# Optimization experiments

Hardware: AMD Instinct MI355X
Metric: run time of the kernel (lower is better)

The kernel has to match this reference:

```python
import jax, jax.numpy as jnp
import numpy as np

TAU = 1.0
K_TAU = 1.0
MAX_K = 64


def setup_inputs() -> dict:
    key = jax.random.key(0)
    ks = jax.random.split(key, 6)
    B, S, D, H = 8, 4096, 1024, 2048
    token_embeddings = jax.random.normal(ks[0], (B, S, D), dtype=jnp.float32)
    W1 = jax.random.normal(ks[1], (D, H), dtype=jnp.float32) * (1.0 / np.sqrt(D))
    b1 = jnp.zeros((H,), dtype=jnp.float32)
    W2 = jax.random.normal(ks[2], (H, 1), dtype=jnp.float32) * (1.0 / np.sqrt(H))
    b2 = jnp.zeros((1,), dtype=jnp.float32)
    k_logits = jax.random.normal(ks[3], (MAX_K,), dtype=jnp.float32) * 0.02
    return {"token_embeddings": token_embeddings, "W1": W1, "b1": b1,
            "W2": W2, "b2": b2, "k_logits": k_logits}


def _gumbel(rng, shape):
    u = jax.random.uniform(rng, shape, minval=1e-08, maxval=1.0 - 1e-08)
    return -jnp.log(-jnp.log(u))


def reference(token_embeddings, W1, b1, W2, b2, k_logits):
    B, S, D = token_embeddings.shape
    # scorer: Dense -> relu -> Dense(1), squeeze -> [B, S]
    h = jax.nn.relu(jnp.einsum('bsd,dh->bsh', token_embeddings, W1) + b1)
    importance_logits = (jnp.einsum('bsh,ho->bso', h, W2) + b2)[..., 0]

    rng = jax.random.key(42)  # training rng
    rng1, rng2 = jax.random.split(rng)

    # learnable-k selection (training branch)
    k_gumbel = _gumbel(rng1, k_logits.shape)
    k_soft = jax.nn.softmax((k_logits + k_gumbel) / K_TAU)
    expected_k = jnp.sum(k_soft * jnp.arange(1, MAX_K + 1, dtype=k_soft.dtype))
    k_selected = jnp.argmax(k_soft) + 1  # traced int scalar

    # gumbel-softmax hard top-k over tokens
    perturbed = importance_logits + _gumbel(rng2, importance_logits.shape)
    soft_mask = jax.nn.softmax(perturbed / TAU, axis=-1)  # [B, S]
    # rank of each token (0 = smallest); top-k == rank >= S - k
    rank = jnp.argsort(jnp.argsort(soft_mask, axis=-1), axis=-1)
    hard_mask = (rank >= S - k_selected).astype(soft_mask.dtype)
    selection_mask = jax.lax.stop_gradient(hard_mask - soft_mask) + soft_mask

    filtered_embeddings = token_embeddings * selection_mask[..., None]
    return filtered_embeddings, selection_mask, expected_k
```

## Files before the change

kernel.cpp:

```cpp
#include <hip/hip_runtime.h>
#include <stdint.h>

#define B_BATCH 8
#define S_SEQ   4096
#define D_DIM   1024
#define H_DIM   2048
#define M_TOK   (B_BATCH * S_SEQ)
#define MAXK    64
#define NSPLIT  2

typedef unsigned int u32;
typedef unsigned short u16;
typedef unsigned long long u64;
typedef __attribute__((ext_vector_type(8))) short short8;
typedef __attribute__((ext_vector_type(4))) float f32x4;

#define GLOBAL_AS __attribute__((address_space(1)))
#define LDS_AS    __attribute__((address_space(3)))


#define TF_ROUND(x0, x1, r) { x0 += x1; x1 = ((x1 << r) | (x1 >> (32 - r))); x1 ^= x0; }

__device__ __forceinline__ void tf2x32(u32 k0, u32 k1, u32 x0, u32 x1, u32& o0, u32& o1) {
  u32 k2 = k0 ^ k1 ^ 0x1BD11BDAu;
  x0 += k0; x1 += k1;
  TF_ROUND(x0, x1, 13) TF_ROUND(x0, x1, 15) TF_ROUND(x0, x1, 26) TF_ROUND(x0, x1, 6)
  x0 += k1; x1 += k2 + 1u;
  TF_ROUND(x0, x1, 17) TF_ROUND(x0, x1, 29) TF_ROUND(x0, x1, 16) TF_ROUND(x0, x1, 24)
  x0 += k2; x1 += k0 + 2u;
  TF_ROUND(x0, x1, 13) TF_ROUND(x0, x1, 15) TF_ROUND(x0, x1, 26) TF_ROUND(x0, x1, 6)
  x0 += k0; x1 += k1 + 3u;
  TF_ROUND(x0, x1, 17) TF_ROUND(x0, x1, 29) TF_ROUND(x0, x1, 16) TF_ROUND(x0, x1, 24)
  x0 += k1; x1 += k2 + 4u;
  TF_ROUND(x0, x1, 13) TF_ROUND(x0, x1, 15) TF_ROUND(x0, x1, 26) TF_ROUND(x0, x1, 6)
  x0 += k2; x1 += k0 + 5u;
  o0 = x0; o1 = x1;
}

__device__ __forceinline__ void jax_subkeys(u32& r1a, u32& r1b, u32& r2a, u32& r2b) {
  tf2x32(0u, 42u, 0u, 0u, r1a, r1b);
  tf2x32(0u, 42u, 0u, 1u, r2a, r2b);
}

__device__ __forceinline__ u32 jax_bits32(u32 ka, u32 kb, u32 i) {
  u32 o0, o1;
  tf2x32(ka, kb, 0u, i, o0, o1);
  return o0 ^ o1;
}

__device__ __forceinline__ float jax_uniform_from_bits(u32 bits) {
  float f = __uint_as_float((bits >> 9) | 0x3f800000u) - 1.0f;
  float r = f + 1e-8f;
  return fmaxf(1e-8f, r);
}

__device__ __forceinline__ float gumbel_from_bits(u32 bits) {
  float u = jax_uniform_from_bits(bits);
  return -logf(-logf(u));
}

__device__ __forceinline__ u32 ordf(float v) {
  u32 b = __float_as_uint(v);
  return (b & 0x80000000u) ? ~b : (b | 0x80000000u);
}

__device__ __forceinline__ u64 shflx64(u64 v, int m) {
  unsigned lo = (unsigned)v, hi = (unsigned)(v >> 32);
  lo = (unsigned)__shfl_xor((int)lo, m);
  hi = (unsigned)__shfl_xor((int)hi, m);
  return ((u64)hi << 32) | lo;
}


__device__ __forceinline__ u16 f2bf_rn(float x) {
  u32 u = __float_as_uint(x);
  u32 r = u + 0x7fffu + ((u >> 16) & 1u);
  return (u16)(r >> 16);
}

__device__ __forceinline__ void split1(float x, u16& h, u16& lo) {
  h = f2bf_rn(x);
  float hf = __uint_as_float(((u32)h) << 16);
  lo = f2bf_rn(x - hf);
}


__global__ __launch_bounds__(256) void prep_a_img(const float* __restrict__ x,
                                                  u16* __restrict__ img) {
  const u32 t = blockIdx.x * 256 + threadIdx.x;
  const int idx512 = (int)(t & 511);
  const int u1 = (int)((t >> 9) & 1);
  const int kt = (int)((t >> 10) & 31);
  const int mt = (int)(t >> 15);
  const int w = idx512 >> 6, l = idx512 & 63;
  const int sig = w * 16 + (l >> 2);
  const int r = sig + (sig & 64) + u1 * 64;
  const int c = (l & 3) ^ ((sig >> 1) & 3);
  const float* src = x + (size_t)(mt * 256 + r) * D_DIM + kt * 32 + c * 8;
  float4 v0 = *(const float4*)src;
  float4 v1 = *(const float4*)(src + 4);
  union { u16 a[8]; short8 v; } H, L;
  split1(v0.x, H.a[0], L.a[0]); split1(v0.y, H.a[1], L.a[1]);
  split1(v0.z, H.a[2], L.a[2]); split1(v0.w, H.a[3], L.a[3]);
  split1(v1.x, H.a[4], L.a[4]); split1(v1.y, H.a[5], L.a[5]);
  split1(v1.z, H.a[6], L.a[6]); split1(v1.w, H.a[7], L.a[7]);
  u16* dhi = img + (size_t)(mt * 32 + kt) * 16384 + u1 * 4096 + idx512 * 8;
  *(short8*)dhi = H.v;
  *(short8*)(dhi + 8192) = L.v;
}

__global__ __launch_bounds__(256) void prep_b_img(const float* __restrict__ W1,
                                                  u16* __restrict__ img) {
  __shared__ float tile[64][33];
  const int tid = threadIdx.x;
  const int bid = blockIdx.x;
  const int n0 = (bid & 63) * 32, k0 = (bid >> 6) * 64;
  const int tx = tid & 31, ty = tid >> 5;
  #pragma unroll
  for (int rr = 0; rr < 8; ++rr)
    tile[ty + rr * 8][tx] = W1[(size_t)(k0 + ty + rr * 8) * H_DIM + n0 + tx];
  __syncthreads();
  const int nc = tid & 31, c8 = tid >> 5;
  const int ktl = c8 >> 2, cc = c8 & 3;
  const int n = n0 + nc;
  const int nyb = n >> 10, t8 = (n >> 8) & 3, rr_ = n & 255;
  const int hiU = rr_ >> 7;
  const int sig = rr_ & 127;
  const int w_ = sig >> 4;
  const int lpos = (sig & 15) * 4 + (cc ^ ((sig >> 1) & 3));
  const int kt = (k0 >> 5) + ktl;
  union { u16 a[8]; short8 v; } H, L;
  #pragma unroll
  for (int j = 0; j < 8; ++j)
    split1(tile[ktl * 32 + cc * 8 + j][nc], H.a[j], L.a[j]);
  u16* d = img + (size_t)nyb * 2097152 + (size_t)(t8 * 32 + kt) * 16384
               + hiU * 4096 + w_ * 512 + lpos * 8;
  *(short8*)d = H.v;
  *(short8*)(d + 8192) = L.v;
}


__device__ __forceinline__ void stage16(const u16* g, u16* l) {
  __builtin_amdgcn_global_load_lds((const GLOBAL_AS u32*)g, (LDS_AS u32*)l, 16, 0, 0);
}

#define WAITV(N) asm volatile("s_waitcnt vmcnt(" #N ")" ::: "memory")
#define FENCE()  asm volatile("" ::: "memory")

__global__ __launch_bounds__(512, 2) void scorer_mfma256(
    const u16* __restrict__ Aimg, const u16* __restrict__ Bimg,
    const float* __restrict__ b1, const float* __restrict__ W2,
    float* __restrict__ pl) {
  extern __shared__ u16 smem[];
  float* red = (float*)(smem + 65536);

  const int tid = threadIdx.x;
  const int w = tid >> 6, l = tid & 63;
  const int wm = w >> 2, wn = w & 3;

  const int b = blockIdx.x;
  const int xcd = b & 7;
  const int nyb = xcd & 1;
  const int mt = (b >> 3) * 4 + (xcd >> 1);
  const int m0 = mt * 256;

  const u16* const Amt = Aimg + (size_t)mt * 524288;
  const u16* const Bny = Bimg + (size_t)nyb * 2097152;
  const int lane16 = w * 512 + l * 8;
  u16* const ldsw = smem + w * 512;

#define ST_A(T, U) stage16(Amt + (size_t)((((T) & 31) * 16384) + (U) * 4096) + lane16, \
                           ldsw + (((T) & 1) << 15) + (U) * 4096)
#define ST_B(T, U) stage16(Bny + (size_t)(((((T) >> 5) * 32 + ((T) & 31)) * 16384) + (U) * 4096) + lane16, \
                           ldsw + (((T) & 1) << 15) + 16384 + (U) * 4096)

  int a_off[8], b_off[4];
  #pragma unroll
  for (int mf = 0; mf < 8; ++mf) {
    int slot = wm * 64 + (mf & 3) * 16 + (l & 15);
    a_off[mf] = ((mf >> 2) * 4096) + slot * 32 + (((l >> 4) ^ ((slot >> 1) & 3)) << 3);
  }
  #pragma unroll
  for (int nf = 0; nf < 4; ++nf) {
    int r = wn * 64 + nf * 16 + (l & 15);
    b_off[nf] = r * 32 + (((l >> 4) ^ ((r >> 1) & 3)) << 3);
  }

  f32x4 acc[8][4];
  #pragma unroll
  for (int mf = 0; mf < 8; ++mf)
    #pragma unroll
    for (int nf = 0; nf < 4; ++nf) acc[mf][nf] = (f32x4){0.f, 0.f, 0.f, 0.f};

  const u16* const B0 = smem;
  const u16* const B1 = smem + 32768;
  short8 ah0, ah1, al0, al1, bh[4], bl[4];

#define LDA(BASE, MF) \
  ah0 = *(const short8*)((BASE) + a_off[MF]); \
  ah1 = *(const short8*)((BASE) + a_off[(MF) + 1]); \
  al0 = *(const short8*)((BASE) + 8192 + a_off[MF]); \
  al1 = *(const short8*)((BASE) + 8192 + a_off[(MF) + 1])

#define LDB(BASE) \
  { _Pragma("unroll") \
    for (int nf = 0; nf < 4; ++nf) { \
      bh[nf] = *(const short8*)((BASE) + 16384 + b_off[nf]); \
      bl[nf] = *(const short8*)((BASE) + 24576 + b_off[nf]); \
    } }

#define MMA2(MF) \
  __builtin_amdgcn_s_setprio(1); \
  { _Pragma("unroll") \
    for (int nf = 0; nf < 4; ++nf) { \
      acc[MF][nf] = __builtin_amdgcn_mfma_f32_16x16x32_bf16(ah0, bh[nf], acc[MF][nf], 0, 0, 0); \
      acc[MF][nf] = __builtin_amdgcn_mfma_f32_16x16x32_bf16(ah0, bl[nf], acc[MF][nf], 0, 0, 0); \
      acc[MF][nf] = __builtin_amdgcn_mfma_f32_16x16x32_bf16(al0, bh[nf], acc[MF][nf], 0, 0, 0); \
      acc[(MF) + 1][nf] = __builtin_amdgcn_mfma_f32_16x16x32_bf16(ah1, bh[nf], acc[(MF) + 1][nf], 0, 0, 0); \
      acc[(MF) + 1][nf] = __builtin_amdgcn_mfma_f32_16x16x32_bf16(ah1, bl[nf], acc[(MF) + 1][nf], 0, 0, 0); \
      acc[(MF) + 1][nf] = __builtin_amdgcn_mfma_f32_16x16x32_bf16(al1, bh[nf], acc[(MF) + 1][nf], 0, 0, 0); \
    } } \
  __builtin_amdgcn_s_setprio(0)

  ST_B(0, 0); ST_B(0, 1); ST_B(0, 2); ST_B(0, 3);
  ST_A(0, 0); ST_A(0, 2); ST_A(0, 1); ST_A(0, 3);
  ST_B(1, 0); ST_B(1, 1); ST_B(1, 2); ST_B(1, 3);
  ST_A(1, 0); ST_A(1, 2);
  WAITV(8);
  __builtin_amdgcn_s_barrier();
  FENCE();

  for (int it = 0; it < 64; ++it) {
    const bool last = (it == 63);
    const int T1 = 2 * it + 1, T2 = 2 * it + 2, T3 = 2 * it + 3;

    LDB(B0); LDA(B0, 0);
    ST_A(T1, 1); ST_A(T1, 3);
    MMA2(0);
    __builtin_amdgcn_s_barrier(); FENCE();
    LDA(B0, 2);
    if (!last) { ST_B(T2, 0); ST_B(T2, 1); }
    MMA2(2);
    if (last) { WAITV(8); } else { WAITV(10); }
    __builtin_amdgcn_s_barrier(); FENCE();
    LDA(B0, 4);
    if (!last) { ST_B(T2, 2); ST_B(T2, 3); }
    MMA2(4);
    __builtin_amdgcn_s_barrier(); FENCE();
    LDA(B0, 6);
    if (!last) { ST_A(T2, 0); ST_A(T2, 2); }
    MMA2(6);
    if (last) { WAITV(2); } else { WAITV(8); }
    __builtin_amdgcn_s_barrier(); FENCE();
    LDB(B1); LDA(B1, 0);
    if (!last) { ST_A(T2, 1); ST_A(T2, 3); }
    MMA2(0);
    __builtin_amdgcn_s_barrier(); FENCE();
    LDA(B1, 2);
    if (!last) { ST_B(T3, 0); ST_B(T3, 1); }
    MMA2(2);
    if (last) { WAITV(0); } else { WAITV(10); }
    __builtin_amdgcn_s_barrier(); FENCE();
    LDA(B1, 4);
    if (!last) { ST_B(T3, 2); ST_B(T3, 3); }
    MMA2(4);
    __builtin_amdgcn_s_barrier(); FENCE();
    LDA(B1, 6);
    if (!last) { ST_A(T3, 0); ST_A(T3, 2); }
    MMA2(6);

    if ((it & 15) == 15) {
      const int t8 = it >> 4;
      const int nb = nyb * 1024 + t8 * 256 + wn * 64 + (l & 15);
      float b1v[4], w2v[4];
      #pragma unroll
      for (int nf = 0; nf < 4; ++nf) { b1v[nf] = b1[nb + nf * 16]; w2v[nf] = W2[nb + nf * 16]; }
      #pragma unroll
      for (int mf = 0; mf < 8; ++mf)
        #pragma unroll
        for (int r = 0; r < 4; ++r) {
          float p = 0.f;
          #pragma unroll
          for (int nf = 0; nf < 4; ++nf)
            p += fmaxf(acc[mf][nf][r] + b1v[nf], 0.f) * w2v[nf];
          p += __shfl_xor(p, 1); p += __shfl_xor(p, 2);
          p += __shfl_xor(p, 4); p += __shfl_xor(p, 8);
          if ((l & 15) == 0) {
            float* rp = red + ((wm * 128 + mf * 16 + (l >> 4) * 4 + r) << 2) + wn;
            if (t8 == 0) *rp = p; else *rp += p;
          }
        }
      #pragma unroll
      for (int mf = 0; mf < 8; ++mf)
        #pragma unroll
        for (int nf = 0; nf < 4; ++nf) acc[mf][nf] = (f32x4){0.f, 0.f, 0.f, 0.f};
    }

    WAITV(8);
    __builtin_amdgcn_s_barrier(); FENCE();
  }

  __syncthreads();
  if (tid < 256) {
    const float* rp = red + (tid << 2);
    pl[(size_t)nyb * M_TOK + m0 + tid] = rp[0] + rp[1] + rp[2] + rp[3];
  }
}


__global__ __launch_bounds__(256) void scorer_kernel(
    const float* __restrict__ emb, const float* __restrict__ W1,
    const float* __restrict__ b1, const float* __restrict__ W2,
    const float* __restrict__ b2, float* __restrict__ pert) {
  __shared__ float As[16][68];
  __shared__ float Bs[16][132];
  __shared__ float red[64][17];

  const int tid = threadIdx.x;
  const int tx = tid & 15;
  const int ty = tid >> 4;
  const int m0 = blockIdx.x * 64;
  const int at = tid >> 2;
  const int ac = (tid & 3) << 2;
  const int br = tid >> 4;
  const int bc = (tid & 15) << 3;

  float logit[4] = {0.f, 0.f, 0.f, 0.f};

  for (int n0 = 0; n0 < H_DIM; n0 += 128) {
    float acc[4][8];
    #pragma unroll
    for (int i = 0; i < 4; i++)
      #pragma unroll
      for (int j = 0; j < 8; j++) acc[i][j] = 0.f;

    for (int k0 = 0; k0 < D_DIM; k0 += 16) {
      float4 av  = *(const float4*)(emb + (size_t)(m0 + at) * D_DIM + (k0 + ac));
      float4 bv0 = *(const float4*)(W1 + (size_t)(k0 + br) * H_DIM + (n0 + bc));
      float4 bv1 = *(const float4*)(W1 + (size_t)(k0 + br) * H_DIM + (n0 + bc) + 4);
      __syncthreads();
      As[ac + 0][at] = av.x; As[ac + 1][at] = av.y;
      As[ac + 2][at] = av.z; As[ac + 3][at] = av.w;
      *(float4*)&Bs[br][bc]     = bv0;
      *(float4*)&Bs[br][bc + 4] = bv1;
      __syncthreads();
      #pragma unroll
      for (int k = 0; k < 16; k++) {
        float4 a   = *(const float4*)&As[k][ty << 2];
        float4 b0  = *(const float4*)&Bs[k][tx << 3];
        float4 b1v = *(const float4*)&Bs[k][(tx << 3) + 4];
        float aa[4] = {a.x, a.y, a.z, a.w};
        float bb[8] = {b0.x, b0.y, b0.z, b0.w, b1v.x, b1v.y, b1v.z, b1v.w};
        #pragma unroll
        for (int i = 0; i < 4; i++)
          #pragma unroll
          for (int j = 0; j < 8; j++)
            acc[i][j] = fmaf(aa[i], bb[j], acc[i][j]);
      }
    }
    float4 c0 = *(const float4*)(b1 + n0 + (tx << 3));
    float4 c1 = *(const float4*)(b1 + n0 + (tx << 3) + 4);
    float4 w0 = *(const float4*)(W2 + n0 + (tx << 3));
    float4 w1 = *(const float4*)(W2 + n0 + (tx << 3) + 4);
    float cb[8] = {c0.x, c0.y, c0.z, c0.w, c1.x, c1.y, c1.z, c1.w};
    float wb[8] = {w0.x, w0.y, w0.z, w0.w, w1.x, w1.y, w1.z, w1.w};
    #pragma unroll
    for (int i = 0; i < 4; i++)
      #pragma unroll
      for (int j = 0; j < 8; j++) {
        float h = fmaxf(acc[i][j] + cb[j], 0.f);
        logit[i] = fmaf(h, wb[j], logit[i]);
      }
  }

  __syncthreads();
  #pragma unroll
  for (int i = 0; i < 4; i++) red[(ty << 2) + i][tx] = logit[i];
  __syncthreads();

  if (tid < 64) {
    float s = 0.f;
    #pragma unroll
    for (int x = 0; x < 16; x++) s += red[tid][x];
    s += b2[0];
    int t = m0 + tid;
    u32 r1a, r1b, r2a, r2b;
    jax_subkeys(r1a, r1b, r2a, r2b);
    pert[t] = s + gumbel_from_bits(jax_bits32(r2a, r2b, (u32)t));
  }
}


template <bool FROM_PL>
__device__ __forceinline__ void topk_body(const float* kl, const float* pl,
                                          const float* b2, float* mask,
                                          float* expk) {
  const int r = blockIdx.x;
  const int tid = threadIdx.x;
  const int w = tid >> 6, l = tid & 63;
  __shared__ int ksel_sh;
  __shared__ int cnt[2][4];

  u32 r1a, r1b, r2a, r2b;
  jax_subkeys(r1a, r1b, r2a, r2b);

  if (tid < 64) {
    float p = kl[l] + gumbel_from_bits(jax_bits32(r1a, r1b, (u32)l));
    u64 kkey = ((u64)ordf(p) << 32) | (unsigned)(63 - l);
    #pragma unroll
    for (int off = 32; off >= 1; off >>= 1) {
      u64 o = shflx64(kkey, off);
      if (o > kkey) kkey = o;
    }
    if (l == 0) ksel_sh = 64 - (int)(kkey & 0xffffffffu);
    if (r == 0) {
      float m = p;
      #pragma unroll
      for (int off = 32; off >= 1; off >>= 1) m = fmaxf(m, __shfl_xor(m, off));
      float e = expf(p - m);
      float s = e;
      #pragma unroll
      for (int off = 32; off >= 1; off >>= 1) s += __shfl_xor(s, off);
      float v = (e / s) * (float)(l + 1);
      #pragma unroll
      for (int off = 32; off >= 1; off >>= 1) v += __shfl_xor(v, off);
      if (l == 0) expk[0] = v;
    }
  }
  __syncthreads();
  const int k = ksel_sh;
  const float b2v = FROM_PL ? b2[0] : 0.f;

  u64 keys[16];
  #pragma unroll
  for (int j = 0; j < 16; j++) {
    int s = tid + (j << 8);
    int t = (r << 12) + s;
    float v;
    if (FROM_PL) {
      float acc = pl[t];
      #pragma unroll
      for (int q = 1; q < NSPLIT; ++q) acc += pl[(size_t)q * M_TOK + t];
      v = acc + b2v + gumbel_from_bits(jax_bits32(r2a, r2b, (u32)t));
    } else {
      v = mask[t];
    }
    keys[j] = ((u64)ordf(v) << 12) | (unsigned)s;
  }

  u64 lo = 0ull, hi = (1ull << 44) - 1ull;
  int it = 0;
  while (lo < hi) {
    const u64 mid = (lo + hi + 1ull) >> 1;
    int c = 0;
    #pragma unroll
    for (int j = 0; j < 16; j++) c += (keys[j] >= mid) ? 1 : 0;
    #pragma unroll
    for (int off = 32; off >= 1; off >>= 1) c += __shfl_xor(c, off);
    const int buf = it & 1;
    if (l == 0) cnt[buf][w] = c;
    __syncthreads();
    const int tot = cnt[buf][0] + cnt[buf][1] + cnt[buf][2] + cnt[buf][3];
    if (tot >= k) lo = mid; else hi = mid - 1ull;
    ++it;
  }
  const u64 thresh = lo;

  #pragma unroll
  for (int j = 0; j < 16; j++) {
    int s = tid + (j << 8);
    mask[(r << 12) + s] = (keys[j] >= thresh) ? 1.0f : 0.0f;
  }
}

__global__ __launch_bounds__(256) void topk_pl_kernel(const float* __restrict__ kl,
                                                      const float* __restrict__ pl,
                                                      const float* __restrict__ b2,
                                                      float* __restrict__ mask,
                                                      float* __restrict__ expk) {
  topk_body<true>(kl, pl, b2, mask, expk);
}

__global__ __launch_bounds__(256) void topk_kernel(const float* __restrict__ kl,
                                                   float* __restrict__ mask,
                                                   float* __restrict__ expk) {
  topk_body<false>(kl, nullptr, nullptr, mask, expk);
}


__global__ __launch_bounds__(256) void filter_kernel(const float* __restrict__ emb,
                                                     const float* __restrict__ mask,
                                                     float* __restrict__ out) {
  const int t = blockIdx.x;
  const float mk = mask[t];
  const size_t base = (size_t)t * D_DIM + ((size_t)threadIdx.x << 2);
  float4 v = *(const float4*)(emb + base);
  *(float4*)(out + base) = make_float4(v.x * mk, v.y * mk, v.z * mk, v.w * mk);
}


extern "C" void kernel_launch(void* const* d_in, const int* in_sizes, int n_in,
                              void* d_out, int out_size, void* d_ws, size_t ws_size,
                              hipStream_t stream) {
  const float* emb = (const float*)d_in[0];
  const float* W1  = (const float*)d_in[1];
  const float* b1  = (const float*)d_in[2];
  const float* W2  = (const float*)d_in[3];
  const float* b2  = (const float*)d_in[4];
  const float* kl  = (const float*)d_in[5];
  float* out  = (float*)d_out;
  float* mask = out + (size_t)M_TOK * D_DIM;
  float* expk = mask + M_TOK;

  const size_t ws_need = (size_t)H_DIM * D_DIM * 2 * 2 + (size_t)NSPLIT * M_TOK * 4;

  if (ws_size >= ws_need) {
    u16* Aimg = (u16*)d_out;
    u16* Bimg = (u16*)d_ws;
    float* pl = (float*)(Bimg + (size_t)2 * H_DIM * D_DIM);

    static bool attr_done = false;
    if (!attr_done) {
      hipFuncSetAttribute(reinterpret_cast<const void*>(scorer_mfma256),
                          hipFuncAttributeMaxDynamicSharedMemorySize, 135168);
      attr_done = true;
    }

    prep_a_img<<<16384, 256, 0, stream>>>(emb, Aimg);
    prep_b_img<<<1024, 256, 0, stream>>>(W1, Bimg);
    scorer_mfma256<<<256, 512, 135168, stream>>>(Aimg, Bimg, b1, W2, pl);
    topk_pl_kernel<<<B_BATCH, 256, 0, stream>>>(kl, pl, b2, mask, expk);
  } else {
    scorer_kernel<<<M_TOK / 64, 256, 0, stream>>>(emb, W1, b1, W2, b2, mask);
    topk_kernel<<<B_BATCH, 256, 0, stream>>>(kl, mask, expk);
  }

  filter_kernel<<<M_TOK, 256, 0, stream>>>(emb, mask, out);
}
```

Measured before the change: 587.5 us.

## Switch scorer GEMM from 16x16x32 to 32x32x16 bf16 MFMA tiles

Replaces the 16x16x32 bf16 MFMA fragments with 32x32x16 MFMA, reorganising per-wave A/B LDS offsets, register fragments, accumulators (f32x16) and the fused relu·W2 epilogue reduction to match the new output layout. Larger MFMA tiles reduce LDS fragment reads per FLOP and instruction issue overhead. The three-term bf16 split (hi*hi, hi*lo, lo*hi) is kept. It risks bank conflicts under the new swizzle mapping and changes the pipelining granularity between the staging and barrier steps.

```diff
diff --git a/kernel.cpp b/kernel.cpp
--- a/kernel.cpp
+++ b/kernel.cpp
@@ -14,6 +14,7 @@
 typedef unsigned long long u64;
 typedef __attribute__((ext_vector_type(8))) short short8;
 typedef __attribute__((ext_vector_type(4))) float f32x4;
+typedef __attribute__((ext_vector_type(16))) float f32x16;
 
 #define GLOBAL_AS __attribute__((address_space(1)))
 #define LDS_AS    __attribute__((address_space(3)))
@@ -174,52 +175,69 @@
 #define ST_B(T, U) stage16(Bny + (size_t)(((((T) >> 5) * 32 + ((T) & 31)) * 16384) + (U) * 4096) + lane16, \
                            ldsw + (((T) & 1) << 15) + 16384 + (U) * 4096)
 
-  int a_off[8], b_off[4];
-  #pragma unroll
-  for (int mf = 0; mf < 8; ++mf) {
-    int slot = wm * 64 + (mf & 3) * 16 + (l & 15);
-    a_off[mf] = ((mf >> 2) * 4096) + slot * 32 + (((l >> 4) ^ ((slot >> 1) & 3)) << 3);
-  }
-  #pragma unroll
-  for (int nf = 0; nf < 4; ++nf) {
-    int r = wn * 64 + nf * 16 + (l & 15);
-    b_off[nf] = r * 32 + (((l >> 4) ^ ((r >> 1) & 3)) << 3);
-  }
-
-  f32x4 acc[8][4];
-  #pragma unroll
-  for (int mf = 0; mf < 8; ++mf)
-    #pragma unroll
-    for (int nf = 0; nf < 4; ++nf) acc[mf][nf] = (f32x4){0.f, 0.f, 0.f, 0.f};
+  int a_off[4][2], b_off[2][2];
+  #pragma unroll
+  for (int mf = 0; mf < 4; ++mf) {
+    const int slot = wm * 64 + (mf & 1) * 32 + (l & 31);
+    #pragma unroll
+    for (int ks = 0; ks < 2; ++ks) {
+      const int c = ks * 2 + (l >> 5);
+      a_off[mf][ks] = (mf >> 1) * 4096 + slot * 32 + ((c ^ ((slot >> 1) & 3)) << 3);
+    }
+  }
+  #pragma unroll
+  for (int nf = 0; nf < 2; ++nf) {
+    const int slotb = (wn & 1) * 64 + nf * 32 + (l & 31);
+    #pragma unroll
+    for (int ks = 0; ks < 2; ++ks) {
+      const int c = ks * 2 + (l >> 5);
+      b_off[nf][ks] = (wn >> 1) * 4096 + slotb * 32 + ((c ^ ((slotb >> 1) & 3)) << 3);
+    }
+  }
+
+  f32x16 acc[4][2];
+  #pragma unroll
+  for (int mf = 0; mf < 4; ++mf)
+    #pragma unroll
+    for (int nf = 0; nf < 2; ++nf)
+      #pragma unroll
+      for (int r = 0; r < 16; ++r) acc[mf][nf][r] = 0.f;
 
   const u16* const B0 = smem;
   const u16* const B1 = smem + 32768;
-  short8 ah0, ah1, al0, al1, bh[4], bl[4];
+  short8 ah[2], al[2], bh[2][2], bl[2][2];
 
 #define LDA(BASE, MF) \
-  ah0 = *(const short8*)((BASE) + a_off[MF]); \
-  ah1 = *(const short8*)((BASE) + a_off[(MF) + 1]); \
-  al0 = *(const short8*)((BASE) + 8192 + a_off[MF]); \
-  al1 = *(const short8*)((BASE) + 8192 + a_off[(MF) + 1])
+  ah[0] = *(const short8*)((BASE) + a_off[MF][0]); \
+  ah[1] = *(const short8*)((BASE) + a_off[MF][1]); \
+  al[0] = *(const short8*)((BASE) + 8192 + a_off[MF][0]); \
+  al[1] = *(const short8*)((BASE) + 8192 + a_off[MF][1])
 
 #define LDB(BASE) \
   { _Pragma("unroll") \
-    for (int nf = 0; nf < 4; ++nf) { \
-      bh[nf] = *(const short8*)((BASE) + 16384 + b_off[nf]); \
-      bl[nf] = *(const short8*)((BASE) + 24576 + b_off[nf]); \
+    for (int nf = 0; nf < 2; ++nf) { \
+      bh[nf][0] = *(const short8*)((BASE) + 16384 + b_off[nf][0]); \
+      bh[nf][1] = *(const short8*)((BASE) + 16384 + b_off[nf][1]); \
+      bl[nf][0] = *(const short8*)((BASE) + 24576 + b_off[nf][0]); \
+      bl[nf][1] = *(const short8*)((BASE) + 24576 + b_off[nf][1]); \
     } }
 
-#define MMA2(MF) \
+#define MFMA32(A, Bv, C) __builtin_amdgcn_mfma_f32_32x32x16_bf16(A, Bv, C, 0, 0, 0)
+
+#define MMA1(MF) \
   __builtin_amdgcn_s_setprio(1); \
-  { _Pragma("unroll") \
-    for (int nf = 0; nf < 4; ++nf) { \
-      acc[MF][nf] = __builtin_amdgcn_mfma_f32_16x16x32_bf16(ah0, bh[nf], acc[MF][nf], 0, 0, 0); \
-      acc[MF][nf] = __builtin_amdgcn_mfma_f32_16x16x32_bf16(ah0, bl[nf], acc[MF][nf], 0, 0, 0); \
-      acc[MF][nf] = __builtin_amdgcn_mfma_f32_16x16x32_bf16(al0, bh[nf], acc[MF][nf], 0, 0, 0); \
-      acc[(MF) + 1][nf] = __builtin_amdgcn_mfma_f32_16x16x32_bf16(ah1, bh[nf], acc[(MF) + 1][nf], 0, 0, 0); \
-      acc[(MF) + 1][nf] = __builtin_amdgcn_mfma_f32_16x16x32_bf16(ah1, bl[nf], acc[(MF) + 1][nf], 0, 0, 0); \
-      acc[(MF) + 1][nf] = __builtin_amdgcn_mfma_f32_16x16x32_bf16(al1, bh[nf], acc[(MF) + 1][nf], 0, 0, 0); \
-    } } \
+  acc[MF][0] = MFMA32(ah[0], bh[0][0], acc[MF][0]); \
+  acc[MF][1] = MFMA32(ah[0], bh[1][0], acc[MF][1]); \
+  acc[MF][0] = MFMA32(ah[1], bh[0][1], acc[MF][0]); \
+  acc[MF][1] = MFMA32(ah[1], bh[1][1], acc[MF][1]); \
+  acc[MF][0] = MFMA32(ah[0], bl[0][0], acc[MF][0]); \
+  acc[MF][1] = MFMA32(ah[0], bl[1][0], acc[MF][1]); \
+  acc[MF][0] = MFMA32(ah[1], bl[0][1], acc[MF][0]); \
+  acc[MF][1] = MFMA32(ah[1], bl[1][1], acc[MF][1]); \
+  acc[MF][0] = MFMA32(al[0], bh[0][0], acc[MF][0]); \
+  acc[MF][1] = MFMA32(al[0], bh[1][0], acc[MF][1]); \
+  acc[MF][0] = MFMA32(al[1], bh[0][1], acc[MF][0]); \
+  acc[MF][1] = MFMA32(al[1], bh[1][1], acc[MF][1]); \
   __builtin_amdgcn_s_setprio(0)
 
   ST_B(0, 0); ST_B(0, 1); ST_B(0, 2); ST_B(0, 3);
@@ -236,64 +254,64 @@
 
     LDB(B0); LDA(B0, 0);
     ST_A(T1, 1); ST_A(T1, 3);
-    MMA2(0);
+    MMA1(0);
+    __builtin_amdgcn_s_barrier(); FENCE();
+    LDA(B0, 1);
+    if (!last) { ST_B(T2, 0); ST_B(T2, 1); }
+    MMA1(1);
+    if (last) { WAITV(8); } else { WAITV(10); }
     __builtin_amdgcn_s_barrier(); FENCE();
     LDA(B0, 2);
-    if (!last) { ST_B(T2, 0); ST_B(T2, 1); }
-    MMA2(2);
-    if (last) { WAITV(8); } else { WAITV(10); }
-    __builtin_amdgcn_s_barrier(); FENCE();
-    LDA(B0, 4);
     if (!last) { ST_B(T2, 2); ST_B(T2, 3); }
-    MMA2(4);
-    __builtin_amdgcn_s_barrier(); FENCE();
-    LDA(B0, 6);
+    MMA1(2);
+    __builtin_amdgcn_s_barrier(); FENCE();
+    LDA(B0, 3);
     if (!last) { ST_A(T2, 0); ST_A(T2, 2); }
-    MMA2(6);
+    MMA1(3);
     if (last) { WAITV(2); } else { WAITV(8); }
     __builtin_amdgcn_s_barrier(); FENCE();
     LDB(B1); LDA(B1, 0);
     if (!last) { ST_A(T2, 1); ST_A(T2, 3); }
-    MMA2(0);
+    MMA1(0);
+    __builtin_amdgcn_s_barrier(); FENCE();
+    LDA(B1, 1);
+    if (!last) { ST_B(T3, 0); ST_B(T3, 1); }
+    MMA1(1);
+    if (last) { WAITV(0); } else { WAITV(10); }
     __builtin_amdgcn_s_barrier(); FENCE();
     LDA(B1, 2);
-    if (!last) { ST_B(T3, 0); ST_B(T3, 1); }
-    MMA2(2);
-    if (last) { WAITV(0); } else { WAITV(10); }
-    __builtin_amdgcn_s_barrier(); FENCE();
-    LDA(B1, 4);
     if (!last) { ST_B(T3, 2); ST_B(T3, 3); }
-    MMA2(4);
-    __builtin_amdgcn_s_barrier(); FENCE();
-    LDA(B1, 6);
+    MMA1(2);
+    __builtin_amdgcn_s_barrier(); FENCE();
+    LDA(B1, 3);
     if (!last) { ST_A(T3, 0); ST_A(T3, 2); }
-    MMA2(6);
+    MMA1(3);
 
     if ((it & 15) == 15) {
       const int t8 = it >> 4;
-      const int nb = nyb * 1024 + t8 * 256 + wn * 64 + (l & 15);
-      float b1v[4], w2v[4];
-      #pragma unroll
-      for (int nf = 0; nf < 4; ++nf) { b1v[nf] = b1[nb + nf * 16]; w2v[nf] = W2[nb + nf * 16]; }
-      #pragma unroll
-      for (int mf = 0; mf < 8; ++mf)
+      const int nb = nyb * 1024 + t8 * 256 + wn * 64 + (l & 31);
+      float b1v[2], w2v[2];
+      #pragma unroll
+      for (int nf = 0; nf < 2; ++nf) { b1v[nf] = b1[nb + nf * 32]; w2v[nf] = W2[nb + nf * 32]; }
+      #pragma unroll
+      for (int mf = 0; mf < 4; ++mf) {
         #pragma unroll
-        for (int r = 0; r < 4; ++r) {
-          float p = 0.f;
-          #pragma unroll
-          for (int nf = 0; nf < 4; ++nf)
-            p += fmaxf(acc[mf][nf][r] + b1v[nf], 0.f) * w2v[nf];
+        for (int r = 0; r < 16; ++r) {
+          float p = fmaxf(acc[mf][0][r] + b1v[0], 0.f) * w2v[0]
+                  + fmaxf(acc[mf][1][r] + b1v[1], 0.f) * w2v[1];
           p += __shfl_xor(p, 1); p += __shfl_xor(p, 2);
-          p += __shfl_xor(p, 4); p += __shfl_xor(p, 8);
-          if ((l & 15) == 0) {
-            float* rp = red + ((wm * 128 + mf * 16 + (l >> 4) * 4 + r) << 2) + wn;
+          p += __shfl_xor(p, 4); p += __shfl_xor(p, 8); p += __shfl_xor(p, 16);
+          if ((l & 31) == 0) {
+            const int row = wm * 128 + mf * 32 + (r & 3) + 8 * (r >> 2) + ((l >> 5) << 2);
+            float* rp = red + (row << 2) + wn;
             if (t8 == 0) *rp = p; else *rp += p;
           }
         }
-      #pragma unroll
-      for (int mf = 0; mf < 8; ++mf)
         #pragma unroll
-        for (int nf = 0; nf < 4; ++nf) acc[mf][nf] = (f32x4){0.f, 0.f, 0.f, 0.f};
+        for (int nf = 0; nf < 2; ++nf)
+          #pragma unroll
+          for (int r = 0; r < 16; ++r) acc[mf][nf][r] = 0.f;
+      }
     }
 
     WAITV(8);
```

Result: slower. 669.6 us (+14.0%).

## Coarsen MFMA phases to four-fragment quads and remap block-to-XCD tiling

Applied to the files above, without the earlier changes.

Restructures the main loop of the bf16x3 MFMA scorer GEMM from eight two-fragment phases per iteration to four four-fragment phases. This halves the number of barriers per iteration and issues the global-to-LDS stages in larger groups, with adjusted vmcnt waits. It also remaps block indices so each XCD handles a contiguous range of M tiles, covering both N halves, which aims at better L2 reuse of A. In exchange it needs more A-fragment registers and overlaps loads with compute at a coarser grain, which could hurt latency hiding or occupancy.

```diff
diff --git a/kernel.cpp b/kernel.cpp
--- a/kernel.cpp
+++ b/kernel.cpp
@@ -160,8 +160,9 @@
 
   const int b = blockIdx.x;
   const int xcd = b & 7;
-  const int nyb = xcd & 1;
-  const int mt = (b >> 3) * 4 + (xcd >> 1);
+  const int j = b >> 3;
+  const int nyb = j & 1;
+  const int mt = xcd * 16 + (j >> 1);
   const int m0 = mt * 256;
 
   const u16* const Amt = Aimg + (size_t)mt * 524288;
@@ -194,13 +195,21 @@
 
   const u16* const B0 = smem;
   const u16* const B1 = smem + 32768;
-  short8 ah0, ah1, al0, al1, bh[4], bl[4];
-
-#define LDA(BASE, MF) \
-  ah0 = *(const short8*)((BASE) + a_off[MF]); \
-  ah1 = *(const short8*)((BASE) + a_off[(MF) + 1]); \
-  al0 = *(const short8*)((BASE) + 8192 + a_off[MF]); \
-  al1 = *(const short8*)((BASE) + 8192 + a_off[(MF) + 1])
+  short8 ah[4], al[4], bh[4], bl[4];
+
+#define LDA_E(BASE) \
+  { _Pragma("unroll") \
+    for (int i = 0; i < 4; ++i) { \
+      ah[i] = *(const short8*)((BASE) + a_off[i]); \
+      al[i] = *(const short8*)((BASE) + 8192 + a_off[i]); \
+    } }
+
+#define LDA_L(BASE) \
+  { _Pragma("unroll") \
+    for (int i = 0; i < 4; ++i) { \
+      ah[i] = *(const short8*)((BASE) + a_off[4 + i]); \
+      al[i] = *(const short8*)((BASE) + 8192 + a_off[4 + i]); \
+    } }
 
 #define LDB(BASE) \
   { _Pragma("unroll") \
@@ -209,21 +218,21 @@
       bl[nf] = *(const short8*)((BASE) + 24576 + b_off[nf]); \
     } }
 
-#define MMA2(MF) \
+#define MMA_QUAD(MB) \
   __builtin_amdgcn_s_setprio(1); \
   { _Pragma("unroll") \
-    for (int nf = 0; nf < 4; ++nf) { \
-      acc[MF][nf] = __builtin_amdgcn_mfma_f32_16x16x32_bf16(ah0, bh[nf], acc[MF][nf], 0, 0, 0); \
-      acc[MF][nf] = __builtin_amdgcn_mfma_f32_16x16x32_bf16(ah0, bl[nf], acc[MF][nf], 0, 0, 0); \
-      acc[MF][nf] = __builtin_amdgcn_mfma_f32_16x16x32_bf16(al0, bh[nf], acc[MF][nf], 0, 0, 0); \
-      acc[(MF) + 1][nf] = __builtin_amdgcn_mfma_f32_16x16x32_bf16(ah1, bh[nf], acc[(MF) + 1][nf], 0, 0, 0); \
-      acc[(MF) + 1][nf] = __builtin_amdgcn_mfma_f32_16x16x32_bf16(ah1, bl[nf], acc[(MF) + 1][nf], 0, 0, 0); \
-      acc[(MF) + 1][nf] = __builtin_amdgcn_mfma_f32_16x16x32_bf16(al1, bh[nf], acc[(MF) + 1][nf], 0, 0, 0); \
-    } } \
+    for (int mf = 0; mf < 4; ++mf) \
+      _Pragma("unroll") \
+      for (int nf = 0; nf < 4; ++nf) { \
+        acc[(MB) + mf][nf] = __builtin_amdgcn_mfma_f32_16x16x32_bf16(ah[mf], bh[nf], acc[(MB) + mf][nf], 0, 0, 0); \
+        acc[(MB) + mf][nf] = __builtin_amdgcn_mfma_f32_16x16x32_bf16(ah[mf], bl[nf], acc[(MB) + mf][nf], 0, 0, 0); \
+        acc[(MB) + mf][nf] = __builtin_amdgcn_mfma_f32_16x16x32_bf16(al[mf], bh[nf], acc[(MB) + mf][nf], 0, 0, 0); \
+      } } \
   __builtin_amdgcn_s_setprio(0)
 
   ST_B(0, 0); ST_B(0, 1); ST_B(0, 2); ST_B(0, 3);
-  ST_A(0, 0); ST_A(0, 2); ST_A(0, 1); ST_A(0, 3);
+  ST_A(0, 0); ST_A(0, 2);
+  ST_A(0, 1); ST_A(0, 3);
   ST_B(1, 0); ST_B(1, 1); ST_B(1, 2); ST_B(1, 3);
   ST_A(1, 0); ST_A(1, 2);
   WAITV(8);
@@ -234,40 +243,27 @@
     const bool last = (it == 63);
     const int T1 = 2 * it + 1, T2 = 2 * it + 2, T3 = 2 * it + 3;
 
-    LDB(B0); LDA(B0, 0);
+    LDB(B0); LDA_E(B0);
     ST_A(T1, 1); ST_A(T1, 3);
-    MMA2(0);
+    MMA_QUAD(0);
+    WAITV(8);
     __builtin_amdgcn_s_barrier(); FENCE();
-    LDA(B0, 2);
-    if (!last) { ST_B(T2, 0); ST_B(T2, 1); }
-    MMA2(2);
-    if (last) { WAITV(8); } else { WAITV(10); }
-    __builtin_amdgcn_s_barrier(); FENCE();
-    LDA(B0, 4);
-    if (!last) { ST_B(T2, 2); ST_B(T2, 3); }
-    MMA2(4);
-    __builtin_amdgcn_s_barrier(); FENCE();
-    LDA(B0, 6);
-    if (!last) { ST_A(T2, 0); ST_A(T2, 2); }
-    MMA2(6);
+
+    LDA_L(B0);
+    if (!last) { ST_B(T2, 0); ST_B(T2, 1); ST_B(T2, 2); ST_B(T2, 3); ST_A(T2, 0); ST_A(T2, 2); }
+    MMA_QUAD(4);
     if (last) { WAITV(2); } else { WAITV(8); }
     __builtin_amdgcn_s_barrier(); FENCE();
-    LDB(B1); LDA(B1, 0);
+
+    LDB(B1); LDA_E(B1);
     if (!last) { ST_A(T2, 1); ST_A(T2, 3); }
-    MMA2(0);
+    MMA_QUAD(0);
+    if (last) { WAITV(0); } else { WAITV(8); }
     __builtin_amdgcn_s_barrier(); FENCE();
-    LDA(B1, 2);
-    if (!last) { ST_B(T3, 0); ST_B(T3, 1); }
-    MMA2(2);
-    if (last) { WAITV(0); } else { WAITV(10); }
-    __builtin_amdgcn_s_barrier(); FENCE();
-    LDA(B1, 4);
-    if (!last) { ST_B(T3, 2); ST_B(T3, 3); }
-    MMA2(4);
-    __builtin_amdgcn_s_barrier(); FENCE();
-    LDA(B1, 6);
-    if (!last) { ST_A(T3, 0); ST_A(T3, 2); }
-    MMA2(6);
+
+    LDA_L(B1);
+    if (!last) { ST_B(T3, 0); ST_B(T3, 1); ST_B(T3, 2); ST_B(T3, 3); ST_A(T3, 0); ST_A(T3, 2); }
+    MMA_QUAD(4);
 
     if ((it & 15) == 15) {
       const int t8 = it >> 4;
@@ -296,7 +292,7 @@
         for (int nf = 0; nf < 4; ++nf) acc[mf][nf] = (f32x4){0.f, 0.f, 0.f, 0.f};
     }
 
-    WAITV(8);
+    if (!last) WAITV(8);
     __builtin_amdgcn_s_barrier(); FENCE();
   }
 
```

After: 602.4 us. 2.5% more time.
